# Performance work log

Measured on AMD Instinct MI355X. Metric: run time of the kernel, lower is better.

Reference implementation:

```python
import jax, jax.numpy as jnp
import numpy as np

NEG = -9e15
ALPHA = 0.2  # LeakyReLU slope


def xavier(key, shape, gain=1.414):
    fan_in, fan_out = shape[-2], shape[-1]
    bound = gain * np.sqrt(6.0 / (fan_in + fan_out))
    return jax.random.uniform(key, shape, jnp.float32, -bound, bound)


def setup_inputs() -> dict:
    key = jax.random.key(0)
    ks = jax.random.split(key, 8)
    N, D_IN, HID, OUT, H = 4096, 128, 64, 64, 4
    x = jax.random.normal(ks[0], (N, D_IN), jnp.float32)
    adj = jax.random.randint(ks[1], (N, N), 0, 2, jnp.int32)
    # layer 0: in=D_IN, out=HID, heads=H
    W0 = xavier(ks[2], (H, D_IN, HID))
    a0 = xavier(ks[3], (H, 2 * HID, 1))
    # layer 1: in=HID*H, out=HID, heads=H
    W1 = xavier(ks[4], (H, HID * H, HID))
    a1 = xavier(ks[5], (H, 2 * HID, 1))
    # layer 2: in=HID*H, out=OUT, heads=1
    W2 = xavier(ks[6], (1, HID * H, OUT))
    a2 = xavier(ks[7], (1, 2 * OUT, 1))
    return {"x": x, "adj": adj, "W0": W0, "a0": a0, "W1": W1, "a1": a1, "W2": W2, "a2": a2}


def gat_layer(x, adj_mask, W, a):
    # x: [N, D], W: [H, D, O], a: [H, 2O, 1]
    O = W.shape[-1]
    h = jnp.einsum('nd,hdo->hno', x, W)                      # [H, N, O]
    a_l, a_r = a[:, :O, 0], a[:, O:, 0]                      # [H, O] each
    e_l = jnp.einsum('hno,ho->hn', h, a_l)                   # a^T[Wh_i||Wh_j] split
    e_r = jnp.einsum('hno,ho->hn', h, a_r)
    e = e_l[:, :, None] + e_r[:, None, :]                    # [H, N, N]
    e = jnp.where(e > 0, e, ALPHA * e)                       # LeakyReLU
    att = jnp.where(adj_mask[None], e, NEG)
    att = jax.nn.softmax(att, axis=-1)                       # dropout skipped (eval)
    out = jnp.einsum('hnm,hmo->hno', att, h)                 # [H, N, O]
    N = x.shape[0]
    return out.transpose(1, 0, 2).reshape(N, -1)             # [N, H*O]


def reference(x, adj, W0, a0, W1, a1, W2, a2):
    adj_mask = adj > 0
    h = gat_layer(x, adj_mask, W0, a0)
    h = jax.nn.elu(h)
    h = gat_layer(h, adj_mask, W1, a1)
    h = jax.nn.elu(h)
    h = gat_layer(h, adj_mask, W2, a2)
    return h
```

## Files before the change

kernel.cpp:

```cpp
#include <hip/hip_runtime.h>

#define LOG2E 1.4426950408889634f

typedef float  f32x4 __attribute__((ext_vector_type(4)));
typedef int    i32x4 __attribute__((ext_vector_type(4)));
typedef short  s16x8 __attribute__((ext_vector_type(8)));

static __device__ __forceinline__ float exp2_fast(float x) {
#if __has_builtin(__builtin_amdgcn_exp2f)
    return __builtin_amdgcn_exp2f(x);
#else
    return exp2f(x);
#endif
}
static __device__ __forceinline__ unsigned short bf16_rne(float f) {
    unsigned u = __float_as_uint(f);
    u += 0x7FFFu + ((u >> 16) & 1u);
    return (unsigned short)(u >> 16);
}

__global__ __launch_bounds__(256) void conv_x(
    const float* __restrict__ xf, unsigned short* __restrict__ xc)
{
    int i = blockIdx.x * 256 + threadIdx.x;
    xc[i] = bf16_rne(xf[i]);
}

__global__ __launch_bounds__(256) void prep_kernel(
    const float* __restrict__ W0, const float* __restrict__ W1,
    const float* __restrict__ W2,
    unsigned short* __restrict__ W0t, unsigned short* __restrict__ W1t,
    unsigned short* __restrict__ W2t)
{
    int gid = blockIdx.x * 256 + threadIdx.x;
    if (gid < 32768) {
        int h = gid >> 13, d = (gid >> 6) & 127, o = gid & 63;
        W0t[(h * 64 + o) * 128 + d] = bf16_rne(W0[gid]);
    } else if (gid < 98304) {
        int g = gid - 32768;
        int h = g >> 14, d = (g >> 6) & 255, o = g & 63;
        W1t[(h * 64 + o) * 256 + d] = bf16_rne(W1[g]);
    } else if (gid < 114688) {
        int g = gid - 98304;
        int d = g >> 6, o = g & 63;
        W2t[o * 256 + d] = bf16_rne(W2[g]);
    }
}

__global__ __launch_bounds__(256) void mk_bits(
    const int* __restrict__ adj, unsigned long long* __restrict__ bits)
{
    int idx = blockIdx.x * 256 + threadIdx.x;
    unsigned long long m = __ballot(adj[idx] != 0);
    if ((idx & 63) == 0) bits[idx >> 6] = m;
}

__global__ __launch_bounds__(256) void gemm_elr(
    const unsigned short* __restrict__ X, int K,
    const unsigned short* __restrict__ Wt,
    const float* __restrict__ a,
    unsigned short* __restrict__ hT,
    float* __restrict__ el2, float* __restrict__ er2)
{
    const int lane = threadIdx.x & 63, w = threadIdx.x >> 6;
    const int c = lane & 15, q = lane >> 4;
    const int h = blockIdx.y;
    const int nb = blockIdx.x * 64 + w * 16;
    const unsigned short* xrow = X + (size_t)(nb + c) * K + q * 8;
    const unsigned short* wb   = Wt + ((size_t)h * 64 + c) * K + q * 8;

    f32x4 acc[4] = {{0,0,0,0},{0,0,0,0},{0,0,0,0},{0,0,0,0}};
    for (int kk = 0; kk < K; kk += 32) {
        s16x8 af = *(const s16x8*)(xrow + kk);
#pragma unroll
        for (int j = 0; j < 4; ++j) {
            s16x8 bf = *(const s16x8*)(wb + (size_t)(j * 16) * K + kk);
            acc[j] = __builtin_amdgcn_mfma_f32_16x16x32_bf16(af, bf, acc[j], 0, 0, 0);
        }
    }
#pragma unroll
    for (int j = 0; j < 4; ++j) {
        unsigned d0 = (unsigned)bf16_rne(acc[j][0]) | ((unsigned)bf16_rne(acc[j][1]) << 16);
        unsigned d1 = (unsigned)bf16_rne(acc[j][2]) | ((unsigned)bf16_rne(acc[j][3]) << 16);
        unsigned short* dst = hT + ((size_t)h * 64 + j * 16 + c) * 4096 + nb + q * 4;
        ((unsigned*)dst)[0] = d0;
        ((unsigned*)dst)[1] = d1;
    }
    const float* ab = a + h * 128;
    float elr[4] = {0,0,0,0}, err[4] = {0,0,0,0};
#pragma unroll
    for (int j = 0; j < 4; ++j) {
        float al = ab[j * 16 + c];
        float ar = ab[64 + j * 16 + c];
#pragma unroll
        for (int r = 0; r < 4; ++r) {
            elr[r] = fmaf(al, acc[j][r], elr[r]);
            err[r] = fmaf(ar, acc[j][r], err[r]);
        }
    }
#pragma unroll
    for (int m = 1; m <= 8; m <<= 1) {
#pragma unroll
        for (int r = 0; r < 4; ++r) {
            elr[r] += __shfl_xor(elr[r], m, 64);
            err[r] += __shfl_xor(err[r], m, 64);
        }
    }
    if (c == 0) {
#pragma unroll
        for (int r = 0; r < 4; ++r) {
            int n = nb + q * 4 + r;
            el2[h * 4096 + n] = elr[r] * LOG2E;
            er2[h * 4096 + n] = err[r] * LOG2E;
        }
    }
}

__global__ __launch_bounds__(256) void hmax_kernel(
    const float* __restrict__ er2, float* __restrict__ Mx)
{
    __shared__ float red[4];
    const int h = blockIdx.x, tid = threadIdx.x;
    float m = -3.0e38f;
#pragma unroll
    for (int i = 0; i < 16; ++i)
        m = fmaxf(m, er2[h * 4096 + i * 256 + tid]);
#pragma unroll
    for (int s = 1; s <= 32; s <<= 1)
        m = fmaxf(m, __shfl_xor(m, s, 64));
    if ((tid & 63) == 0) red[tid >> 6] = m;
    __syncthreads();
    if (tid == 0) {
        float r = fmaxf(fmaxf(red[0], red[1]), fmaxf(red[2], red[3]));
        Mx[h] = r;
    }
}

__global__ __launch_bounds__(256) void att_kernel(
    const unsigned short* __restrict__ hT,
    const float* __restrict__ el2g, const float* __restrict__ er2g,
    const float* __restrict__ Mx,
    const unsigned long long* __restrict__ bits,
    float* __restrict__ accP, float* __restrict__ lP,
    int H, int KPS, int HO)
{
    __shared__ unsigned short ldsH[64 * 264];
    __shared__ float ldsE[256];
    const int tid = threadIdx.x;
    const int lane = tid & 63, w = tid >> 6;
    const int c = lane & 15, q = lane >> 4, q8 = q * 8;
    const int h = blockIdx.y, ks = blockIdx.z;
    const int nb = blockIdx.x * 64 + w * 16;
    const int rowA = nb + c;

    float M2 = Mx[h];
    float e2 = el2g[h * 4096 + rowA];
    float xx = e2 + M2;
    float C2 = fmaxf(xx, 0.2f * xx);
    const float elA = e2 - C2;
    const float elB = fmaf(0.2f, e2, -C2);

    const char* bitrow = (const char*)bits + (size_t)rowA * 512 + (size_t)(KPS >> 3) * ks;

    s16x8 ones = {0,0,0,0,0,0,0,0};
    if (c == 0) {
#pragma unroll
        for (int i = 0; i < 8; ++i) ones[i] = (short)0x3F80;
    }
    f32x4 acc[4] = {{0,0,0,0},{0,0,0,0},{0,0,0,0},{0,0,0,0}};
    f32x4 accl = {0,0,0,0};

    const unsigned short* hTh = hT + (size_t)h * 64 * 4096;
    const float* erh = er2g + h * 4096;
    const int tiles = KPS >> 8;

    for (int t = 0; t < tiles; ++t) {
        const int mabs = ks * KPS + t * 256;
#pragma unroll
        for (int i = 0; i < 8; ++i) {
            int cidx = i * 256 + tid;
            int o = cidx >> 5, seg = cidx & 31;
            i32x4 v = *(const i32x4*)(hTh + (size_t)o * 4096 + mabs + seg * 8);
            *(i32x4*)(ldsH + o * 264 + seg * 8) = v;
        }
        if (tid < 64)
            *(f32x4*)(ldsE + tid * 4) = *(const f32x4*)(erh + mabs + tid * 4);
        __syncthreads();

        i32x4 b0 = *(const i32x4*)(bitrow + t * 32);
        i32x4 b1 = *(const i32x4*)(bitrow + t * 32 + 16);
        int bw[8] = {b0[0], b0[1], b0[2], b0[3], b1[0], b1[1], b1[2], b1[3]};

#pragma unroll
        for (int cc = 0; cc < 8; ++cc) {
            const int kl = cc * 32 + q8;
            f32x4 ea = *(const f32x4*)(ldsE + kl);
            f32x4 eb = *(const f32x4*)(ldsE + kl + 4);
            const unsigned word = (unsigned)bw[cc];
            unsigned pd[4];
#pragma unroll
            for (int jj = 0; jj < 4; ++jj) {
                float er0 = (jj < 2) ? ea[2 * jj]     : eb[2 * jj - 4];
                float er1 = (jj < 2) ? ea[2 * jj + 1] : eb[2 * jj - 3];
                float s0 = fminf(fmaxf(elA + er0, fmaf(0.2f, er0, elB)), 0.f);
                float s1 = fminf(fmaxf(elA + er1, fmaf(0.2f, er1, elB)), 0.f);
                float p0 = exp2_fast(s0);
                float p1 = exp2_fast(s1);
                unsigned m0 = (unsigned)(-(int)((word >> (q8 + 2 * jj)) & 1u));
                unsigned m1 = (unsigned)(-(int)((word >> (q8 + 2 * jj + 1)) & 1u));
                unsigned u0 = __float_as_uint(p0) & m0;
                unsigned u1 = __float_as_uint(p1) & m1;
                pd[jj] = (u0 >> 16) | (u1 & 0xFFFF0000u);
            }
            union { unsigned u[4]; s16x8 s; } afu;
            afu.u[0] = pd[0]; afu.u[1] = pd[1]; afu.u[2] = pd[2]; afu.u[3] = pd[3];
            s16x8 af = afu.s;
            const unsigned short* lb = ldsH + c * 264 + kl;
#pragma unroll
            for (int j = 0; j < 4; ++j) {
                s16x8 bf = *(const s16x8*)(lb + (size_t)(j * 16) * 264);
                acc[j] = __builtin_amdgcn_mfma_f32_16x16x32_bf16(af, bf, acc[j], 0, 0, 0);
            }
            accl = __builtin_amdgcn_mfma_f32_16x16x32_bf16(af, ones, accl, 0, 0, 0);
        }
        __syncthreads();
    }
    float ls[4];
#pragma unroll
    for (int r = 0; r < 4; ++r) ls[r] = __shfl(accl[r], lane & 48, 64);

    float* ap = accP + ((size_t)ks * 4096 + nb + q * 4) * HO + h * 64 + c;
#pragma unroll
    for (int r = 0; r < 4; ++r)
#pragma unroll
        for (int j = 0; j < 4; ++j)
            ap[(size_t)r * HO + j * 16] = acc[j][r];
    if (c == 0) {
#pragma unroll
        for (int r = 0; r < 4; ++r)
            lP[((size_t)ks * H + h) * 4096 + nb + q * 4 + r] = ls[r];
    }
}

__global__ __launch_bounds__(256) void comb_kernel(
    const float* __restrict__ accP, const float* __restrict__ lP,
    unsigned short* __restrict__ outb, float* __restrict__ outf,
    int KS, int H, int lgHO, int do_elu)
{
    const int idx = blockIdx.x * 256 + threadIdx.x;
    const int HO = 1 << lgHO;
    const int n = idx >> lgHO, col = idx & (HO - 1), h = col >> 6;
    float s = 0.f, l = 0.f;
    for (int ks = 0; ks < KS; ++ks) {
        s += accP[((size_t)ks * 4096 + n) * HO + col];
        l += lP[((size_t)ks * H + h) * 4096 + n];
    }
    float v = s / l;
    if (do_elu && v < 0.f) v = exp2_fast(v * LOG2E) - 1.f;
    if (outf) outf[idx] = v;
    else      outb[idx] = bf16_rne(v);
}

extern "C" void kernel_launch(void* const* d_in, const int* in_sizes, int n_in,
                              void* d_out, int out_size, void* d_ws, size_t ws_size,
                              hipStream_t stream)
{
    (void)in_sizes; (void)n_in; (void)out_size; (void)ws_size;
    const float* x   = (const float*)d_in[0];
    const int*   adj = (const int*)d_in[1];
    const float* W0  = (const float*)d_in[2];
    const float* a0  = (const float*)d_in[3];
    const float* W1  = (const float*)d_in[4];
    const float* a1  = (const float*)d_in[5];
    const float* W2  = (const float*)d_in[6];
    const float* a2  = (const float*)d_in[7];

    char* p = (char*)d_ws;
    unsigned long long* bits = (unsigned long long*)(p + 0x000000);
    unsigned short* hT  = (unsigned short*)(p + 0x200000);
    unsigned short* X12 = (unsigned short*)(p + 0x400000);
    unsigned short* Xc  = (unsigned short*)(p + 0x600000);
    unsigned short* W0t = (unsigned short*)(p + 0x700000);
    unsigned short* W1t = (unsigned short*)(p + 0x710000);
    unsigned short* W2t = (unsigned short*)(p + 0x730000);
    float*    el2  = (float*)(p + 0x738000);
    float*    er2  = (float*)(p + 0x748000);
    float*    Mx   = (float*)(p + 0x758000);
    float*    accP = (float*)(p + 0x760000);
    float*    lP   = (float*)(p + 0xF60000);

    conv_x<<<2048, 256, 0, stream>>>(x, Xc);
    prep_kernel<<<448, 256, 0, stream>>>(W0, W1, W2, W0t, W1t, W2t);
    mk_bits<<<65536, 256, 0, stream>>>(adj, bits);

    gemm_elr<<<dim3(64, 4), 256, 0, stream>>>(Xc, 128, W0t, a0, hT, el2, er2);
    hmax_kernel<<<4, 256, 0, stream>>>(er2, Mx);
    att_kernel<<<dim3(64, 4, 2), 256, 0, stream>>>(hT, el2, er2, Mx, bits, accP, lP, 4, 2048, 256);
    comb_kernel<<<4096, 256, 0, stream>>>(accP, lP, X12, nullptr, 2, 4, 8, 1);

    gemm_elr<<<dim3(64, 4), 256, 0, stream>>>(X12, 256, W1t, a1, hT, el2, er2);
    hmax_kernel<<<4, 256, 0, stream>>>(er2, Mx);
    att_kernel<<<dim3(64, 4, 2), 256, 0, stream>>>(hT, el2, er2, Mx, bits, accP, lP, 4, 2048, 256);
    comb_kernel<<<4096, 256, 0, stream>>>(accP, lP, X12, nullptr, 2, 4, 8, 1);

    gemm_elr<<<dim3(64, 1), 256, 0, stream>>>(X12, 256, W2t, a2, hT, el2, er2);
    hmax_kernel<<<1, 256, 0, stream>>>(er2, Mx);
    att_kernel<<<dim3(64, 1, 4), 256, 0, stream>>>(hT, el2, er2, Mx, bits, accP, lP, 1, 1024, 64);
    comb_kernel<<<1024, 256, 0, stream>>>(accP, lP, nullptr, (float*)d_out, 4, 1, 6, 0);
}
```

Baseline: 249.0 us.

## Factor attention exp per row/column, fuse prep kernels, atomic head max

Rewrites the leaky-relu softmax weight as max(A_i*exp2(er_j-M), B_i*exp2(0.2*(er_j-M))), so the exponentials are computed once per column tile and once per row instead of once per element. The inner loop then needs only multiplies and a max. The three prep kernels are merged into one launch, the separate head-max kernel is replaced by an atomicMax on an order-preserving uint key inside gemm_elr, and the LDS padding is replaced with an XOR swizzle. Mask extraction and bf16 packing now use the sbfe and perm builtins. The risks are possible precision differences from computing the weight as a product of exponentials, and added atomic contention.

```diff
diff --git a/kernel.cpp b/kernel.cpp
--- a/kernel.cpp
+++ b/kernel.cpp
@@ -5,6 +5,7 @@
 typedef float  f32x4 __attribute__((ext_vector_type(4)));
 typedef int    i32x4 __attribute__((ext_vector_type(4)));
 typedef short  s16x8 __attribute__((ext_vector_type(8)));
+typedef unsigned long long u64x2 __attribute__((ext_vector_type(2)));
 
 static __device__ __forceinline__ float exp2_fast(float x) {
 #if __has_builtin(__builtin_amdgcn_exp2f)
@@ -18,41 +19,62 @@
     u += 0x7FFFu + ((u >> 16) & 1u);
     return (unsigned short)(u >> 16);
 }
-
-__global__ __launch_bounds__(256) void conv_x(
-    const float* __restrict__ xf, unsigned short* __restrict__ xc)
-{
-    int i = blockIdx.x * 256 + threadIdx.x;
-    xc[i] = bf16_rne(xf[i]);
-}
-
-__global__ __launch_bounds__(256) void prep_kernel(
+static __device__ __forceinline__ int sbfe1(unsigned w, int pos) {
+#if __has_builtin(__builtin_amdgcn_sbfe)
+    return __builtin_amdgcn_sbfe((int)w, pos, 1);
+#else
+    return (int)(w << (31 - pos)) >> 31;
+#endif
+}
+static __device__ __forceinline__ unsigned pack_hi16(unsigned u1, unsigned u0) {
+#if __has_builtin(__builtin_amdgcn_perm)
+    return __builtin_amdgcn_perm(u1, u0, 0x07060302u);
+#else
+    return (u0 >> 16) | (u1 & 0xFFFF0000u);
+#endif
+}
+
+__global__ __launch_bounds__(256) void prep_all(
+    const float* __restrict__ xf, const int* __restrict__ adj,
     const float* __restrict__ W0, const float* __restrict__ W1,
     const float* __restrict__ W2,
+    unsigned short* __restrict__ xc, unsigned long long* __restrict__ bits,
     unsigned short* __restrict__ W0t, unsigned short* __restrict__ W1t,
-    unsigned short* __restrict__ W2t)
-{
-    int gid = blockIdx.x * 256 + threadIdx.x;
-    if (gid < 32768) {
-        int h = gid >> 13, d = (gid >> 6) & 127, o = gid & 63;
-        W0t[(h * 64 + o) * 128 + d] = bf16_rne(W0[gid]);
-    } else if (gid < 98304) {
-        int g = gid - 32768;
-        int h = g >> 14, d = (g >> 6) & 255, o = g & 63;
-        W1t[(h * 64 + o) * 256 + d] = bf16_rne(W1[g]);
-    } else if (gid < 114688) {
-        int g = gid - 98304;
-        int d = g >> 6, o = g & 63;
-        W2t[o * 256 + d] = bf16_rne(W2[g]);
-    }
-}
-
-__global__ __launch_bounds__(256) void mk_bits(
-    const int* __restrict__ adj, unsigned long long* __restrict__ bits)
-{
-    int idx = blockIdx.x * 256 + threadIdx.x;
-    unsigned long long m = __ballot(adj[idx] != 0);
-    if ((idx & 63) == 0) bits[idx >> 6] = m;
+    unsigned short* __restrict__ W2t, unsigned* __restrict__ MxU)
+{
+    const int b = blockIdx.x, tid = threadIdx.x;
+    if (b < 16384) {
+        const int w = tid >> 6, lane = tid & 63;
+        const int base = b * 1024 + w * 256;
+        unsigned long long m[4];
+#pragma unroll
+        for (int r = 0; r < 4; ++r)
+            m[r] = __ballot(adj[base + r * 64 + lane] != 0);
+        if (lane == 0) {
+            u64x2 lo = {m[0], m[1]}, hi = {m[2], m[3]};
+            *(u64x2*)(bits + (base >> 6))     = lo;
+            *(u64x2*)(bits + (base >> 6) + 2) = hi;
+        }
+    } else if (b < 18432) {
+        int i = (b - 16384) * 256 + tid;
+        xc[i] = bf16_rne(xf[i]);
+    } else {
+        int gid = (b - 18432) * 256 + tid;
+        if (gid < 32768) {
+            int h = gid >> 13, d = (gid >> 6) & 127, o = gid & 63;
+            W0t[(h * 64 + o) * 128 + d] = bf16_rne(W0[gid]);
+        } else if (gid < 98304) {
+            int g = gid - 32768;
+            int h = g >> 14, d = (g >> 6) & 255, o = g & 63;
+            W1t[(h * 64 + o) * 256 + d] = bf16_rne(W1[g]);
+        } else if (gid < 114688) {
+            int g = gid - 98304;
+            int d = g >> 6, o = g & 63;
+            W2t[o * 256 + d] = bf16_rne(W2[g]);
+        } else if (gid < 114700) {
+            MxU[gid - 114688] = 0x007FFFFFu;
+        }
+    }
 }
 
 __global__ __launch_bounds__(256) void gemm_elr(
@@ -60,7 +82,8 @@
     const unsigned short* __restrict__ Wt,
     const float* __restrict__ a,
     unsigned short* __restrict__ hT,
-    float* __restrict__ el2, float* __restrict__ er2)
+    float* __restrict__ el2, float* __restrict__ er2,
+    unsigned* __restrict__ MxU)
 {
     const int lane = threadIdx.x & 63, w = threadIdx.x >> 6;
     const int c = lane & 15, q = lane >> 4;
@@ -114,38 +137,26 @@
             er2[h * 4096 + n] = err[r] * LOG2E;
         }
     }
-}
-
-__global__ __launch_bounds__(256) void hmax_kernel(
-    const float* __restrict__ er2, float* __restrict__ Mx)
-{
-    __shared__ float red[4];
-    const int h = blockIdx.x, tid = threadIdx.x;
-    float m = -3.0e38f;
-#pragma unroll
-    for (int i = 0; i < 16; ++i)
-        m = fmaxf(m, er2[h * 4096 + i * 256 + tid]);
-#pragma unroll
-    for (int s = 1; s <= 32; s <<= 1)
-        m = fmaxf(m, __shfl_xor(m, s, 64));
-    if ((tid & 63) == 0) red[tid >> 6] = m;
-    __syncthreads();
-    if (tid == 0) {
-        float r = fmaxf(fmaxf(red[0], red[1]), fmaxf(red[2], red[3]));
-        Mx[h] = r;
+    float mm = fmaxf(fmaxf(err[0], err[1]), fmaxf(err[2], err[3]));
+    mm = fmaxf(mm, __shfl_xor(mm, 16, 64));
+    mm = fmaxf(mm, __shfl_xor(mm, 32, 64));
+    if (lane == 0) {
+        unsigned u = __float_as_uint(mm * LOG2E);
+        unsigned key = (u & 0x80000000u) ? ~u : (u | 0x80000000u);
+        atomicMax(MxU + h, key);
     }
 }
 
 __global__ __launch_bounds__(256) void att_kernel(
     const unsigned short* __restrict__ hT,
     const float* __restrict__ el2g, const float* __restrict__ er2g,
-    const float* __restrict__ Mx,
+    const unsigned* __restrict__ MxU,
     const unsigned long long* __restrict__ bits,
     float* __restrict__ accP, float* __restrict__ lP,
     int H, int KPS, int HO)
 {
-    __shared__ unsigned short ldsH[64 * 264];
-    __shared__ float ldsE[256];
+    __shared__ unsigned short ldsH[64 * 256];
+    __shared__ float ldsE[512];
     const int tid = threadIdx.x;
     const int lane = tid & 63, w = tid >> 6;
     const int c = lane & 15, q = lane >> 4, q8 = q * 8;
@@ -153,12 +164,13 @@
     const int nb = blockIdx.x * 64 + w * 16;
     const int rowA = nb + c;
 
-    float M2 = Mx[h];
+    unsigned kM = MxU[h];
+    float M2 = __uint_as_float((kM & 0x80000000u) ? (kM & 0x7FFFFFFFu) : ~kM);
     float e2 = el2g[h * 4096 + rowA];
     float xx = e2 + M2;
     float C2 = fmaxf(xx, 0.2f * xx);
-    const float elA = e2 - C2;
-    const float elB = fmaf(0.2f, e2, -C2);
+    const float Al = exp2_fast(xx - C2);
+    const float Bl = exp2_fast(fmaf(0.2f, xx, -C2));
 
     const char* bitrow = (const char*)bits + (size_t)rowA * 512 + (size_t)(KPS >> 3) * ks;
 
@@ -181,10 +193,13 @@
             int cidx = i * 256 + tid;
             int o = cidx >> 5, seg = cidx & 31;
             i32x4 v = *(const i32x4*)(hTh + (size_t)o * 4096 + mabs + seg * 8);
-            *(i32x4*)(ldsH + o * 264 + seg * 8) = v;
-        }
-        if (tid < 64)
-            *(f32x4*)(ldsE + tid * 4) = *(const f32x4*)(erh + mabs + tid * 4);
+            *(i32x4*)(ldsH + o * 256 + ((seg ^ (o & 7)) << 3)) = v;
+        }
+        {
+            float er = erh[mabs + tid] - M2;
+            ldsE[2 * tid]     = exp2_fast(er);
+            ldsE[2 * tid + 1] = exp2_fast(0.2f * er);
+        }
         __syncthreads();
 
         i32x4 b0 = *(const i32x4*)(bitrow + t * 32);
@@ -194,31 +209,27 @@
 #pragma unroll
         for (int cc = 0; cc < 8; ++cc) {
             const int kl = cc * 32 + q8;
-            f32x4 ea = *(const f32x4*)(ldsE + kl);
-            f32x4 eb = *(const f32x4*)(ldsE + kl + 4);
+            const f32x4* ep = (const f32x4*)(ldsE + 2 * kl);
+            f32x4 ev0 = ep[0], ev1 = ep[1], ev2 = ep[2], ev3 = ep[3];
             const unsigned word = (unsigned)bw[cc];
             unsigned pd[4];
 #pragma unroll
             for (int jj = 0; jj < 4; ++jj) {
-                float er0 = (jj < 2) ? ea[2 * jj]     : eb[2 * jj - 4];
-                float er1 = (jj < 2) ? ea[2 * jj + 1] : eb[2 * jj - 3];
-                float s0 = fminf(fmaxf(elA + er0, fmaf(0.2f, er0, elB)), 0.f);
-                float s1 = fminf(fmaxf(elA + er1, fmaf(0.2f, er1, elB)), 0.f);
-                float p0 = exp2_fast(s0);
-                float p1 = exp2_fast(s1);
-                unsigned m0 = (unsigned)(-(int)((word >> (q8 + 2 * jj)) & 1u));
-                unsigned m1 = (unsigned)(-(int)((word >> (q8 + 2 * jj + 1)) & 1u));
-                unsigned u0 = __float_as_uint(p0) & m0;
-                unsigned u1 = __float_as_uint(p1) & m1;
-                pd[jj] = (u0 >> 16) | (u1 & 0xFFFF0000u);
+                f32x4 ev = (jj == 0) ? ev0 : (jj == 1) ? ev1 : (jj == 2) ? ev2 : ev3;
+                float p0 = fmaxf(Al * ev[0], Bl * ev[1]);
+                float p1 = fmaxf(Al * ev[2], Bl * ev[3]);
+                unsigned u0 = __float_as_uint(p0) & (unsigned)sbfe1(word, q8 + 2 * jj);
+                unsigned u1 = __float_as_uint(p1) & (unsigned)sbfe1(word, q8 + 2 * jj + 1);
+                pd[jj] = pack_hi16(u1, u0);
             }
             union { unsigned u[4]; s16x8 s; } afu;
             afu.u[0] = pd[0]; afu.u[1] = pd[1]; afu.u[2] = pd[2]; afu.u[3] = pd[3];
             s16x8 af = afu.s;
-            const unsigned short* lb = ldsH + c * 264 + kl;
+            const int klx = kl ^ ((c & 7) << 3);
+            const unsigned short* lb = ldsH + c * 256 + klx;
 #pragma unroll
             for (int j = 0; j < 4; ++j) {
-                s16x8 bf = *(const s16x8*)(lb + (size_t)(j * 16) * 264);
+                s16x8 bf = *(const s16x8*)(lb + (size_t)(j * 16) * 256);
                 acc[j] = __builtin_amdgcn_mfma_f32_16x16x32_bf16(af, bf, acc[j], 0, 0, 0);
             }
             accl = __builtin_amdgcn_mfma_f32_16x16x32_bf16(af, ones, accl, 0, 0, 0);
@@ -285,26 +296,22 @@
     unsigned short* W2t = (unsigned short*)(p + 0x730000);
     float*    el2  = (float*)(p + 0x738000);
     float*    er2  = (float*)(p + 0x748000);
-    float*    Mx   = (float*)(p + 0x758000);
+    unsigned* MxU  = (unsigned*)(p + 0x758000);
     float*    accP = (float*)(p + 0x760000);
     float*    lP   = (float*)(p + 0xF60000);
 
-    conv_x<<<2048, 256, 0, stream>>>(x, Xc);
-    prep_kernel<<<448, 256, 0, stream>>>(W0, W1, W2, W0t, W1t, W2t);
-    mk_bits<<<65536, 256, 0, stream>>>(adj, bits);
-
-    gemm_elr<<<dim3(64, 4), 256, 0, stream>>>(Xc, 128, W0t, a0, hT, el2, er2);
-    hmax_kernel<<<4, 256, 0, stream>>>(er2, Mx);
-    att_kernel<<<dim3(64, 4, 2), 256, 0, stream>>>(hT, el2, er2, Mx, bits, accP, lP, 4, 2048, 256);
+    prep_all<<<18881, 256, 0, stream>>>(x, adj, W0, W1, W2, Xc, bits,
+                                        W0t, W1t, W2t, MxU);
+
+    gemm_elr<<<dim3(64, 4), 256, 0, stream>>>(Xc, 128, W0t, a0, hT, el2, er2, MxU + 0);
+    att_kernel<<<dim3(64, 4, 2), 256, 0, stream>>>(hT, el2, er2, MxU + 0, bits, accP, lP, 4, 2048, 256);
     comb_kernel<<<4096, 256, 0, stream>>>(accP, lP, X12, nullptr, 2, 4, 8, 1);
 
-    gemm_elr<<<dim3(64, 4), 256, 0, stream>>>(X12, 256, W1t, a1, hT, el2, er2);
-    hmax_kernel<<<4, 256, 0, stream>>>(er2, Mx);
-    att_kernel<<<dim3(64, 4, 2), 256, 0, stream>>>(hT, el2, er2, Mx, bits, accP, lP, 4, 2048, 256);
+    gemm_elr<<<dim3(64, 4), 256, 0, stream>>>(X12, 256, W1t, a1, hT, el2, er2, MxU + 4);
+    att_kernel<<<dim3(64, 4, 2), 256, 0, stream>>>(hT, el2, er2, MxU + 4, bits, accP, lP, 4, 2048, 256);
     comb_kernel<<<4096, 256, 0, stream>>>(accP, lP, X12, nullptr, 2, 4, 8, 1);
 
-    gemm_elr<<<dim3(64, 1), 256, 0, stream>>>(X12, 256, W2t, a2, hT, el2, er2);
-    hmax_kernel<<<1, 256, 0, stream>>>(er2, Mx);
-    att_kernel<<<dim3(64, 1, 4), 256, 0, stream>>>(hT, el2, er2, Mx, bits, accP, lP, 1, 1024, 64);
+    gemm_elr<<<dim3(64, 1), 256, 0, stream>>>(X12, 256, W2t, a2, hT, el2, er2, MxU + 8);
+    att_kernel<<<dim3(64, 1, 4), 256, 0, stream>>>(hT, el2, er2, MxU + 8, bits, accP, lP, 1, 1024, 64);
     comb_kernel<<<1024, 256, 0, stream>>>(accP, lP, nullptr, (float*)d_out, 4, 1, 6, 0);
 }
```

Measured after the change: 276.6 us. 11.1% more time.
